# Optimization experiments

Measured on AMD Instinct MI355X. Metric: run time of the kernel, lower is better.

Reference implementation:

```python
import jax, jax.numpy as jnp
import numpy as np

C = 32          # mid_channel / in_channel
B = 8           # batch size (number of scenes)
N = 2_000_000   # total points across batch
BN_EPS = 1e-4   # BatchNorm1d eps from norm_fn


def setup_inputs() -> dict:
    key = jax.random.key(0)
    ks = jax.random.split(key, 8)
    s = 0.05
    return {
        "feats": jax.random.normal(ks[0], (N, C), dtype=jnp.float32),
        "batch_idxs": jnp.sort(jax.random.randint(ks[1], (N,), 0, B, dtype=jnp.int32)),
        "off_w1": jax.random.normal(ks[2], (C, C), dtype=jnp.float32) * s,
        "off_b1": jnp.zeros((C,), jnp.float32),
        "bn_gamma": jnp.ones((C,), jnp.float32),   # set_bn_init fills 1.0
        "bn_beta": jnp.zeros((C,), jnp.float32),   # set_bn_init fills 0.0
        "off_w2": jax.random.normal(ks[3], (C, 3), dtype=jnp.float32) * s,
        "off_b2": jnp.zeros((3,), jnp.float32),
        "mask_w1": jax.random.normal(ks[4], (C, C), dtype=jnp.float32) * s,
        "mask_b1": jnp.zeros((C,), jnp.float32),
        "mask_w2": jax.random.normal(ks[5], (C, 1), dtype=jnp.float32) * s,
        "mask_b2": jnp.zeros((1,), jnp.float32),
        "iou_w": jax.random.normal(ks[6], (C, 1), dtype=jnp.float32) * s,
        "iou_b": jnp.zeros((1,), jnp.float32),
    }


def reference(feats, batch_idxs, off_w1, off_b1, bn_gamma, bn_beta, off_w2, off_b2,
              mask_w1, mask_b1, mask_w2, mask_b2, iou_w, iou_b):
    # offset_linear = MLP([C, C, 3], norm_fn=BatchNorm1d): Linear -> BN -> ReLU -> Linear
    h = feats @ off_w1 + off_b1                      # [N, C]
    mu = h.mean(axis=0)
    var = jnp.mean(jnp.square(h - mu), axis=0)       # biased var (torch BN training fwd)
    h = (h - mu) * jax.lax.rsqrt(var + BN_EPS) * bn_gamma + bn_beta
    h = jax.nn.relu(h)
    pt_offsets = h @ off_w2 + off_b2                 # [N, 3]

    # mask_linear = MLP([C, C, 1], norm_fn=None): Linear -> ReLU -> Linear
    m = jax.nn.relu(feats @ mask_w1 + mask_b1)       # [N, C]
    mask_scores = m @ mask_w2 + mask_b2              # [N, 1]

    # global_pool: scatter mean of features over per-batch segments (batch offsets)
    ones = jnp.ones((feats.shape[0],), feats.dtype)
    counts = jax.ops.segment_sum(ones, batch_idxs, num_segments=B)          # [B]
    pooled = jax.ops.segment_sum(feats, batch_idxs, num_segments=B)         # [B, C]
    pooled = pooled / jnp.maximum(counts, 1.0)[:, None]

    # iou_score_linear on the pooled proposal feature
    iou_scores = pooled @ iou_w + iou_b              # [B, 1]
    return pt_offsets, mask_scores, pooled, iou_scores
```

## Files before the change

kernel.cpp:

```cpp
#include <hip/hip_runtime.h>

#define TPB 256

typedef __attribute__((ext_vector_type(8))) short short8;
typedef __attribute__((ext_vector_type(4))) float floatx4;

__device__ __forceinline__ unsigned short bf_trunc(float f){
    union { float f; unsigned u; } c; c.f = f;
    return (unsigned short)(c.u >> 16);
}
__device__ __forceinline__ unsigned short bf_rne(float f){
    union { float f; unsigned u; } c; c.f = f;
    unsigned r = c.u + 0x7fffu + ((c.u >> 16) & 1u);
    return (unsigned short)(r >> 16);
}
__device__ __forceinline__ unsigned pack_bf(float lo, float hi){
    union { float f; unsigned u; } a, b; a.f = lo; b.f = hi;
    return __builtin_amdgcn_perm(b.u, a.u, 0x07060302u);
}

__global__ __launch_bounds__(TPB, 4) void pass1_kernel(
    const float* __restrict__ feats, const int* __restrict__ bidx,
    const float* __restrict__ w1, const float* __restrict__ b1,
    const float* __restrict__ mw1, const float* __restrict__ mb1,
    const float* __restrict__ mw2, const float* __restrict__ mb2,
    float* __restrict__ mask_out,
    float* __restrict__ ws_sum, float* __restrict__ ws_sq,
    float* __restrict__ ws_pool, int N, int B)
{
    __shared__ float s_pool[8][32];
    __shared__ float s_sum[32];
    __shared__ float s_sq[32];
    __shared__ int   s_lb[9];

    const int tid  = threadIdx.x;
    const int lane = tid & 63;
    const int p = lane & 15;
    const int q = lane >> 4;

    if (tid < 32){ s_sum[tid] = 0.f; s_sq[tid] = 0.f; }
    ((float*)s_pool)[tid] = 0.f;
    if (tid <= B){
        int lo = 0, hi = N;
        while (lo < hi){
            const int mid = (lo + hi) >> 1;
            if (bidx[mid] < tid) lo = mid + 1; else hi = mid;
        }
        s_lb[tid] = lo;
    }
    __syncthreads();

    short8 aw0, aw1, am0, am1;
    floatx4 ci_h0, ci_h1, ci_m0, ci_m1;
    float mw2v[8];
#pragma unroll
    for (int j = 0; j < 8; ++j){
        const int k = q * 8 + j;
        aw0[j] = (short)bf_rne(w1 [k * 32 + p]);
        aw1[j] = (short)bf_rne(w1 [k * 32 + 16 + p]);
        am0[j] = (short)bf_rne(mw1[k * 32 + p]);
        am1[j] = (short)bf_rne(mw1[k * 32 + 16 + p]);
    }
#pragma unroll
    for (int r = 0; r < 4; ++r){
        const int c0 = q * 4 + r, c1 = 16 + q * 4 + r;
        ci_h0[r] = b1[c0];  ci_h1[r] = b1[c1];
        ci_m0[r] = mb1[c0]; ci_m1[r] = mb1[c1];
        mw2v[r] = mw2[c0];  mw2v[4 + r] = mw2[c1];
    }
    const float mb2s = mb2[0];

    float hsum[8] = {0,0,0,0,0,0,0,0};
    float hsq [8] = {0,0,0,0,0,0,0,0};
    float pacc[8] = {0,0,0,0,0,0,0,0};

    const int ntiles = (N + 15) >> 4;
    const int nw  = gridDim.x * (TPB / 64);
    const int wid = blockIdx.x * (TPB / 64) + (tid >> 6);

    int curb = 0;
    {
        const int r0 = wid << 4;
        while (curb < B - 1 && r0 >= s_lb[curb + 1]) curb++;
    }
    int lbn = s_lb[curb + 1];

    const size_t dstep = ((size_t)nw) << 9;
    const float* rp = feats + (((size_t)wid) << 9) + (p << 5) + (q << 3);

    floatx4 v0 = {0.f,0.f,0.f,0.f}, v1 = {0.f,0.f,0.f,0.f};
    if (wid < ntiles){
        if (((wid << 4) + p) < N){
            const floatx4* vp = (const floatx4*)rp;
            v0 = vp[0]; v1 = vp[1];
        }
    }

    for (int t = wid; t < ntiles; t += nw){
        floatx4 nv0 = {0.f,0.f,0.f,0.f}, nv1 = {0.f,0.f,0.f,0.f};
        const float* np = rp + dstep;
        if (t + nw < ntiles){
            if ((((t + nw) << 4) + p) < N){
                const floatx4* vp = (const floatx4*)np;
                nv0 = vp[0]; nv1 = vp[1];
            }
        }

        const int r0 = t << 4;
        if (r0 >= lbn){
#pragma unroll
            for (int j = 0; j < 8; ++j){
                if (pacc[j] != 0.f) atomicAdd(&s_pool[curb][q * 8 + j], pacc[j]);
                pacc[j] = 0.f;
            }
            do { curb++; } while (curb < B - 1 && r0 >= s_lb[curb + 1]);
            lbn = s_lb[curb + 1];
        }
        const bool slow = (r0 + 15 >= lbn);

        if (!slow){
            pacc[0] += v0[0]; pacc[1] += v0[1]; pacc[2] += v0[2]; pacc[3] += v0[3];
            pacc[4] += v1[0]; pacc[5] += v1[1]; pacc[6] += v1[2]; pacc[7] += v1[3];
        } else {
            const int row = r0 + p;
            if (row < N){
                int bl = curb;
                for (int c = curb + 1; c < B; ++c) bl += (row >= s_lb[c]);
                atomicAdd(&s_pool[bl][q * 8 + 0], v0[0]);
                atomicAdd(&s_pool[bl][q * 8 + 1], v0[1]);
                atomicAdd(&s_pool[bl][q * 8 + 2], v0[2]);
                atomicAdd(&s_pool[bl][q * 8 + 3], v0[3]);
                atomicAdd(&s_pool[bl][q * 8 + 4], v1[0]);
                atomicAdd(&s_pool[bl][q * 8 + 5], v1[1]);
                atomicAdd(&s_pool[bl][q * 8 + 6], v1[2]);
                atomicAdd(&s_pool[bl][q * 8 + 7], v1[3]);
            }
        }

        short8 bfrag;
        {
            unsigned* bw = (unsigned*)&bfrag;
            bw[0] = pack_bf(v0[0], v0[1]);
            bw[1] = pack_bf(v0[2], v0[3]);
            bw[2] = pack_bf(v1[0], v1[1]);
            bw[3] = pack_bf(v1[2], v1[3]);
        }

        const floatx4 ch0 = __builtin_amdgcn_mfma_f32_16x16x32_bf16(aw0, bfrag, ci_h0, 0, 0, 0);
        const floatx4 ch1 = __builtin_amdgcn_mfma_f32_16x16x32_bf16(aw1, bfrag, ci_h1, 0, 0, 0);
        const floatx4 cm0 = __builtin_amdgcn_mfma_f32_16x16x32_bf16(am0, bfrag, ci_m0, 0, 0, 0);
        const floatx4 cm1 = __builtin_amdgcn_mfma_f32_16x16x32_bf16(am1, bfrag, ci_m1, 0, 0, 0);

        if (!slow){
#pragma unroll
            for (int r = 0; r < 4; ++r){
                const float h0 = ch0[r]; hsum[r]     += h0; hsq[r]     = fmaf(h0, h0, hsq[r]);
                const float h1 = ch1[r]; hsum[4 + r] += h1; hsq[4 + r] = fmaf(h1, h1, hsq[4 + r]);
            }
        } else if (r0 + p < N){
#pragma unroll
            for (int r = 0; r < 4; ++r){
                const float h0 = ch0[r]; hsum[r]     += h0; hsq[r]     = fmaf(h0, h0, hsq[r]);
                const float h1 = ch1[r]; hsum[4 + r] += h1; hsq[4 + r] = fmaf(h1, h1, hsq[4 + r]);
            }
        }

        float tm = 0.f;
#pragma unroll
        for (int r = 0; r < 4; ++r){
            tm = fmaf(fmaxf(cm0[r], 0.f), mw2v[r],     tm);
            tm = fmaf(fmaxf(cm1[r], 0.f), mw2v[4 + r], tm);
        }
        tm += __shfl_xor(tm, 16, 64);
        tm += __shfl_xor(tm, 32, 64);
        if (q == 0 && (r0 + p) < N) mask_out[r0 + p] = tm + mb2s;

        v0 = nv0; v1 = nv1; rp = np;
    }

#pragma unroll
    for (int j = 0; j < 8; ++j){
        if (pacc[j] != 0.f) atomicAdd(&s_pool[curb][q * 8 + j], pacc[j]);
    }
#pragma unroll
    for (int i = 0; i < 8; ++i){
        const int ch = (i >> 2) * 16 + q * 4 + (i & 3);
        atomicAdd(&s_sum[ch], hsum[i]);
        atomicAdd(&s_sq[ch],  hsq[i]);
    }
    __syncthreads();
    if (tid < 32){
        atomicAdd(&ws_sum[tid], s_sum[tid]);
        atomicAdd(&ws_sq[tid],  s_sq[tid]);
    }
    {
        const float pv = ((float*)s_pool)[tid];
        if (pv != 0.f) atomicAdd(&ws_pool[tid], pv);
    }
}

__global__ __launch_bounds__(TPB, 4) void pass2_kernel(
    const float* __restrict__ feats, const int* __restrict__ bidx,
    const float* __restrict__ w1, const float* __restrict__ b1,
    const float* __restrict__ gamma, const float* __restrict__ beta,
    const float* __restrict__ w2, const float* __restrict__ b2,
    const float* __restrict__ iw, const float* __restrict__ ib,
    const float* __restrict__ ws_sum, const float* __restrict__ ws_sq,
    const float* __restrict__ ws_pool,
    float* __restrict__ pt_out, float* __restrict__ pooled_out,
    float* __restrict__ iou_out, int N, int B)
{
    __shared__ float s_sc[32];
    __shared__ float s_bp[32];
    __shared__ float s_pooled[256];
    __shared__ int   s_lb[33];

    const int tid  = threadIdx.x;
    const int lane = tid & 63;
    const int p = lane & 15;
    const int q = lane >> 4;

    if (tid < 32){
        const float invN = 1.f / (float)N;
        const float mu  = ws_sum[tid] * invN;
        const float var = ws_sq[tid] * invN - mu * mu;
        const float s   = gamma[tid] * rsqrtf(var + 1e-4f);
        s_sc[tid] = s;
        s_bp[tid] = (b1[tid] - mu) * s + beta[tid];
    }
    __syncthreads();

    if (blockIdx.x == 0){
        if (tid <= B){
            int lo = 0, hi = N;
            while (lo < hi){
                const int mid = (lo + hi) >> 1;
                if (bidx[mid] < tid) lo = mid + 1; else hi = mid;
            }
            s_lb[tid] = lo;
        }
        __syncthreads();
        if (tid < B * 32){
            const int bb = tid >> 5;
            const float cnt = fmaxf((float)(s_lb[bb + 1] - s_lb[bb]), 1.f);
            const float pv = ws_pool[tid] / cnt;
            s_pooled[tid]   = pv;
            pooled_out[tid] = pv;
        }
        __syncthreads();
        if (tid < B){
            float acc = ib[0];
#pragma unroll
            for (int i = 0; i < 32; ++i) acc = fmaf(s_pooled[tid * 32 + i], iw[i], acc);
            iou_out[tid] = acc;
        }
    }

    short8 pw0, pw1;
    floatx4 pc0, pc1;
    float w2v[24];
    const float sc0 = s_sc[p], sc1 = s_sc[16 + p];
#pragma unroll
    for (int j = 0; j < 8; ++j){
        const int k = q * 8 + j;
        pw0[j] = (short)bf_rne(w1[k * 32 + p]      * sc0);
        pw1[j] = (short)bf_rne(w1[k * 32 + 16 + p] * sc1);
    }
#pragma unroll
    for (int r = 0; r < 4; ++r){
        pc0[r] = s_bp[q * 4 + r];
        pc1[r] = s_bp[16 + q * 4 + r];
    }
#pragma unroll
    for (int i = 0; i < 8; ++i){
        const int ch = (i >> 2) * 16 + q * 4 + (i & 3);
        w2v[i]      = w2[ch * 3 + 0];
        w2v[8 + i]  = w2[ch * 3 + 1];
        w2v[16 + i] = w2[ch * 3 + 2];
    }
    const float b2v0 = b2[0], b2v1 = b2[1], b2v2 = b2[2];

    const int ntiles = (N + 15) >> 4;
    const int nw  = gridDim.x * (TPB / 64);
    const int wid = blockIdx.x * (TPB / 64) + (tid >> 6);

    const size_t dstep = ((size_t)nw) << 9;
    const float* rp = feats + (((size_t)wid) << 9) + (p << 5) + (q << 3);

    floatx4 v0 = {0.f,0.f,0.f,0.f}, v1 = {0.f,0.f,0.f,0.f};
    if (wid < ntiles){
        if (((wid << 4) + p) < N){
            const floatx4* vp = (const floatx4*)rp;
            v0 = vp[0]; v1 = vp[1];
        }
    }

    for (int t = wid; t < ntiles; t += nw){
        floatx4 nv0 = {0.f,0.f,0.f,0.f}, nv1 = {0.f,0.f,0.f,0.f};
        const float* np = rp + dstep;
        if (t + nw < ntiles){
            if ((((t + nw) << 4) + p) < N){
                const floatx4* vp = (const floatx4*)np;
                nv0 = vp[0]; nv1 = vp[1];
            }
        }

        short8 bfrag;
        {
            unsigned* bw = (unsigned*)&bfrag;
            bw[0] = pack_bf(v0[0], v0[1]);
            bw[1] = pack_bf(v0[2], v0[3]);
            bw[2] = pack_bf(v1[0], v1[1]);
            bw[3] = pack_bf(v1[2], v1[3]);
        }

        const floatx4 c0 = __builtin_amdgcn_mfma_f32_16x16x32_bf16(pw0, bfrag, pc0, 0, 0, 0);
        const floatx4 c1 = __builtin_amdgcn_mfma_f32_16x16x32_bf16(pw1, bfrag, pc1, 0, 0, 0);

        float s0 = 0.f, s1 = 0.f, s2 = 0.f;
#pragma unroll
        for (int r = 0; r < 4; ++r){
            const float p0 = fmaxf(c0[r], 0.f);
            const float p1 = fmaxf(c1[r], 0.f);
            s0 = fmaf(p0, w2v[r],      s0); s0 = fmaf(p1, w2v[4 + r],  s0);
            s1 = fmaf(p0, w2v[8 + r],  s1); s1 = fmaf(p1, w2v[12 + r], s1);
            s2 = fmaf(p0, w2v[16 + r], s2); s2 = fmaf(p1, w2v[20 + r], s2);
        }
        s0 += __shfl_xor(s0, 16, 64); s0 += __shfl_xor(s0, 32, 64);
        s1 += __shfl_xor(s1, 16, 64); s1 += __shfl_xor(s1, 32, 64);
        s2 += __shfl_xor(s2, 16, 64); s2 += __shfl_xor(s2, 32, 64);

        const int row = (t << 4) + p;
        if (lane < 48 && row < N){
            float val = (q == 0) ? (s0 + b2v0) : ((q == 1) ? (s1 + b2v1) : (s2 + b2v2));
            pt_out[(size_t)(t << 4) * 3 + p * 3 + q] = val;
        }

        v0 = nv0; v1 = nv1; rp = np;
    }
}

extern "C" void kernel_launch(void* const* d_in, const int* in_sizes, int n_in,
                              void* d_out, int out_size, void* d_ws, size_t ws_size,
                              hipStream_t stream) {
    const float* feats = (const float*)d_in[0];
    const int*   bidx  = (const int*)d_in[1];
    const float* w1    = (const float*)d_in[2];
    const float* b1    = (const float*)d_in[3];
    const float* gamma = (const float*)d_in[4];
    const float* beta  = (const float*)d_in[5];
    const float* w2    = (const float*)d_in[6];
    const float* b2    = (const float*)d_in[7];
    const float* mw1   = (const float*)d_in[8];
    const float* mb1   = (const float*)d_in[9];
    const float* mw2   = (const float*)d_in[10];
    const float* mb2   = (const float*)d_in[11];
    const float* iw    = (const float*)d_in[12];
    const float* ib    = (const float*)d_in[13];

    const int N = in_sizes[0] / 32;
    const int B = (out_size - 4 * N) / 33;

    float* out    = (float*)d_out;
    float* pt     = out;
    float* mask   = out + (size_t)3 * N;
    float* pooled = out + (size_t)4 * N;
    float* iou    = pooled + (size_t)B * 32;

    float* ws      = (float*)d_ws;
    float* ws_sum  = ws;
    float* ws_sq   = ws + 32;
    float* ws_pool = ws + 64;

    hipMemsetAsync(ws, 0, (size_t)(64 + B * 32) * sizeof(float), stream);

    int dev = 0;
    hipGetDevice(&dev);
    hipDeviceProp_t prop;
    hipGetDeviceProperties(&prop, dev);
    int per1 = 0, per2 = 0;
    hipOccupancyMaxActiveBlocksPerMultiprocessor(&per1, pass1_kernel, TPB, 0);
    hipOccupancyMaxActiveBlocksPerMultiprocessor(&per2, pass2_kernel, TPB, 0);
    int g1 = per1 * prop.multiProcessorCount; if (g1 < 256) g1 = 256;
    int g2 = per2 * prop.multiProcessorCount; if (g2 < 256) g2 = 256;

    pass1_kernel<<<g1, TPB, 0, stream>>>(feats, bidx, w1, b1, mw1, mb1, mw2, mb2,
                                         mask, ws_sum, ws_sq, ws_pool, N, B);
    pass2_kernel<<<g2, TPB, 0, stream>>>(feats, bidx, w1, b1, gamma, beta, w2, b2,
                                         iw, ib, ws_sum, ws_sq, ws_pool,
                                         pt, pooled, iou, N, B);
}
```

Measured before the change: 468.0 us.

## Process two 16-row tiles per iteration over contiguous per-wave ranges with fixed grid

Each wave now owns a contiguous range of 32-row pairs instead of grid-striding 16-row tiles, and handles two tiles per loop iteration with eight (pass1) or four (pass2) independent MFMAs. This gives more memory and compute work in flight per iteration and better locality, and the fixed 1024-block grid removes the per-call device property and occupancy queries from the host launch path. Launch bounds drop to 2 blocks per CU to leave room for the extra registers. The cost is fewer resident waves and a grid size no longer tuned to the device.

```diff
diff --git a/kernel.cpp b/kernel.cpp
--- a/kernel.cpp
+++ b/kernel.cpp
@@ -1,14 +1,11 @@
 #include <hip/hip_runtime.h>
 
 #define TPB 256
+#define GRID_BLOCKS 1024
 
 typedef __attribute__((ext_vector_type(8))) short short8;
 typedef __attribute__((ext_vector_type(4))) float floatx4;
 
-__device__ __forceinline__ unsigned short bf_trunc(float f){
-    union { float f; unsigned u; } c; c.f = f;
-    return (unsigned short)(c.u >> 16);
-}
 __device__ __forceinline__ unsigned short bf_rne(float f){
     union { float f; unsigned u; } c; c.f = f;
     unsigned r = c.u + 0x7fffu + ((c.u >> 16) & 1u);
@@ -19,7 +16,7 @@
     return __builtin_amdgcn_perm(b.u, a.u, 0x07060302u);
 }
 
-__global__ __launch_bounds__(TPB, 4) void pass1_kernel(
+__global__ __launch_bounds__(TPB, 2) void pass1_kernel(
     const float* __restrict__ feats, const int* __restrict__ bidx,
     const float* __restrict__ w1, const float* __restrict__ b1,
     const float* __restrict__ mw1, const float* __restrict__ mb1,
@@ -74,39 +71,38 @@
     float hsq [8] = {0,0,0,0,0,0,0,0};
     float pacc[8] = {0,0,0,0,0,0,0,0};
 
-    const int ntiles = (N + 15) >> 4;
+    const int npairs = (N + 31) >> 5;
     const int nw  = gridDim.x * (TPB / 64);
     const int wid = blockIdx.x * (TPB / 64) + (tid >> 6);
+    const int g0  = (int)((long)wid       * npairs / nw);
+    const int g1  = (int)((long)(wid + 1) * npairs / nw);
 
     int curb = 0;
     {
-        const int r0 = wid << 4;
+        const int r0 = g0 << 5;
         while (curb < B - 1 && r0 >= s_lb[curb + 1]) curb++;
     }
     int lbn = s_lb[curb + 1];
 
-    const size_t dstep = ((size_t)nw) << 9;
-    const float* rp = feats + (((size_t)wid) << 9) + (p << 5) + (q << 3);
-
-    floatx4 v0 = {0.f,0.f,0.f,0.f}, v1 = {0.f,0.f,0.f,0.f};
-    if (wid < ntiles){
-        if (((wid << 4) + p) < N){
-            const floatx4* vp = (const floatx4*)rp;
-            v0 = vp[0]; v1 = vp[1];
-        }
-    }
-
-    for (int t = wid; t < ntiles; t += nw){
-        floatx4 nv0 = {0.f,0.f,0.f,0.f}, nv1 = {0.f,0.f,0.f,0.f};
-        const float* np = rp + dstep;
-        if (t + nw < ntiles){
-            if ((((t + nw) << 4) + p) < N){
-                const floatx4* vp = (const floatx4*)np;
-                nv0 = vp[0]; nv1 = vp[1];
-            }
-        }
-
-        const int r0 = t << 4;
+    const float* rp = feats + (((size_t)g0) << 10) + (p << 5) + (q << 3);
+
+    floatx4 vA0 = {0,0,0,0}, vA1 = {0,0,0,0}, vB0 = {0,0,0,0}, vB1 = {0,0,0,0};
+    if (g0 < g1){
+        const int rA = (g0 << 5) + p;
+        if (rA < N){ const floatx4* vp = (const floatx4*)rp; vA0 = vp[0]; vA1 = vp[1]; }
+        if (rA + 16 < N){ const floatx4* vp = (const floatx4*)(rp + 512); vB0 = vp[0]; vB1 = vp[1]; }
+    }
+
+    for (int g = g0; g < g1; ++g){
+        floatx4 nA0 = {0,0,0,0}, nA1 = {0,0,0,0}, nB0 = {0,0,0,0}, nB1 = {0,0,0,0};
+        const float* np = rp + 1024;
+        if (g + 1 < g1){
+            const int rA = ((g + 1) << 5) + p;
+            if (rA < N){ const floatx4* vp = (const floatx4*)np; nA0 = vp[0]; nA1 = vp[1]; }
+            if (rA + 16 < N){ const floatx4* vp = (const floatx4*)(np + 512); nB0 = vp[0]; nB1 = vp[1]; }
+        }
+
+        const int r0 = g << 5;
         if (r0 >= lbn){
 #pragma unroll
             for (int j = 0; j < 8; ++j){
@@ -116,66 +112,101 @@
             do { curb++; } while (curb < B - 1 && r0 >= s_lb[curb + 1]);
             lbn = s_lb[curb + 1];
         }
-        const bool slow = (r0 + 15 >= lbn);
+        const bool slow = (r0 + 31 >= lbn) || (r0 + 31 >= N);
 
         if (!slow){
-            pacc[0] += v0[0]; pacc[1] += v0[1]; pacc[2] += v0[2]; pacc[3] += v0[3];
-            pacc[4] += v1[0]; pacc[5] += v1[1]; pacc[6] += v1[2]; pacc[7] += v1[3];
+            pacc[0] += vA0[0] + vB0[0]; pacc[1] += vA0[1] + vB0[1];
+            pacc[2] += vA0[2] + vB0[2]; pacc[3] += vA0[3] + vB0[3];
+            pacc[4] += vA1[0] + vB1[0]; pacc[5] += vA1[1] + vB1[1];
+            pacc[6] += vA1[2] + vB1[2]; pacc[7] += vA1[3] + vB1[3];
         } else {
-            const int row = r0 + p;
-            if (row < N){
+            const int rA = r0 + p, rB = r0 + 16 + p;
+            if (rA < N){
                 int bl = curb;
-                for (int c = curb + 1; c < B; ++c) bl += (row >= s_lb[c]);
-                atomicAdd(&s_pool[bl][q * 8 + 0], v0[0]);
-                atomicAdd(&s_pool[bl][q * 8 + 1], v0[1]);
-                atomicAdd(&s_pool[bl][q * 8 + 2], v0[2]);
-                atomicAdd(&s_pool[bl][q * 8 + 3], v0[3]);
-                atomicAdd(&s_pool[bl][q * 8 + 4], v1[0]);
-                atomicAdd(&s_pool[bl][q * 8 + 5], v1[1]);
-                atomicAdd(&s_pool[bl][q * 8 + 6], v1[2]);
-                atomicAdd(&s_pool[bl][q * 8 + 7], v1[3]);
-            }
-        }
-
-        short8 bfrag;
+                for (int c = curb + 1; c < B; ++c) bl += (rA >= s_lb[c]);
+                atomicAdd(&s_pool[bl][q * 8 + 0], vA0[0]);
+                atomicAdd(&s_pool[bl][q * 8 + 1], vA0[1]);
+                atomicAdd(&s_pool[bl][q * 8 + 2], vA0[2]);
+                atomicAdd(&s_pool[bl][q * 8 + 3], vA0[3]);
+                atomicAdd(&s_pool[bl][q * 8 + 4], vA1[0]);
+                atomicAdd(&s_pool[bl][q * 8 + 5], vA1[1]);
+                atomicAdd(&s_pool[bl][q * 8 + 6], vA1[2]);
+                atomicAdd(&s_pool[bl][q * 8 + 7], vA1[3]);
+            }
+            if (rB < N){
+                int bl = curb;
+                for (int c = curb + 1; c < B; ++c) bl += (rB >= s_lb[c]);
+                atomicAdd(&s_pool[bl][q * 8 + 0], vB0[0]);
+                atomicAdd(&s_pool[bl][q * 8 + 1], vB0[1]);
+                atomicAdd(&s_pool[bl][q * 8 + 2], vB0[2]);
+                atomicAdd(&s_pool[bl][q * 8 + 3], vB0[3]);
+                atomicAdd(&s_pool[bl][q * 8 + 4], vB1[0]);
+                atomicAdd(&s_pool[bl][q * 8 + 5], vB1[1]);
+                atomicAdd(&s_pool[bl][q * 8 + 6], vB1[2]);
+                atomicAdd(&s_pool[bl][q * 8 + 7], vB1[3]);
+            }
+        }
+
+        short8 bfA, bfB;
         {
-            unsigned* bw = (unsigned*)&bfrag;
-            bw[0] = pack_bf(v0[0], v0[1]);
-            bw[1] = pack_bf(v0[2], v0[3]);
-            bw[2] = pack_bf(v1[0], v1[1]);
-            bw[3] = pack_bf(v1[2], v1[3]);
-        }
-
-        const floatx4 ch0 = __builtin_amdgcn_mfma_f32_16x16x32_bf16(aw0, bfrag, ci_h0, 0, 0, 0);
-        const floatx4 ch1 = __builtin_amdgcn_mfma_f32_16x16x32_bf16(aw1, bfrag, ci_h1, 0, 0, 0);
-        const floatx4 cm0 = __builtin_amdgcn_mfma_f32_16x16x32_bf16(am0, bfrag, ci_m0, 0, 0, 0);
-        const floatx4 cm1 = __builtin_amdgcn_mfma_f32_16x16x32_bf16(am1, bfrag, ci_m1, 0, 0, 0);
+            unsigned* ba = (unsigned*)&bfA;
+            ba[0] = pack_bf(vA0[0], vA0[1]); ba[1] = pack_bf(vA0[2], vA0[3]);
+            ba[2] = pack_bf(vA1[0], vA1[1]); ba[3] = pack_bf(vA1[2], vA1[3]);
+            unsigned* bb = (unsigned*)&bfB;
+            bb[0] = pack_bf(vB0[0], vB0[1]); bb[1] = pack_bf(vB0[2], vB0[3]);
+            bb[2] = pack_bf(vB1[0], vB1[1]); bb[3] = pack_bf(vB1[2], vB1[3]);
+        }
+
+        const floatx4 chA0 = __builtin_amdgcn_mfma_f32_16x16x32_bf16(aw0, bfA, ci_h0, 0, 0, 0);
+        const floatx4 chA1 = __builtin_amdgcn_mfma_f32_16x16x32_bf16(aw1, bfA, ci_h1, 0, 0, 0);
+        const floatx4 cmA0 = __builtin_amdgcn_mfma_f32_16x16x32_bf16(am0, bfA, ci_m0, 0, 0, 0);
+        const floatx4 cmA1 = __builtin_amdgcn_mfma_f32_16x16x32_bf16(am1, bfA, ci_m1, 0, 0, 0);
+        const floatx4 chB0 = __builtin_amdgcn_mfma_f32_16x16x32_bf16(aw0, bfB, ci_h0, 0, 0, 0);
+        const floatx4 chB1 = __builtin_amdgcn_mfma_f32_16x16x32_bf16(aw1, bfB, ci_h1, 0, 0, 0);
+        const floatx4 cmB0 = __builtin_amdgcn_mfma_f32_16x16x32_bf16(am0, bfB, ci_m0, 0, 0, 0);
+        const floatx4 cmB1 = __builtin_amdgcn_mfma_f32_16x16x32_bf16(am1, bfB, ci_m1, 0, 0, 0);
 
         if (!slow){
 #pragma unroll
             for (int r = 0; r < 4; ++r){
-                const float h0 = ch0[r]; hsum[r]     += h0; hsq[r]     = fmaf(h0, h0, hsq[r]);
-                const float h1 = ch1[r]; hsum[4 + r] += h1; hsq[4 + r] = fmaf(h1, h1, hsq[4 + r]);
-            }
-        } else if (r0 + p < N){
-#pragma unroll
-            for (int r = 0; r < 4; ++r){
-                const float h0 = ch0[r]; hsum[r]     += h0; hsq[r]     = fmaf(h0, h0, hsq[r]);
-                const float h1 = ch1[r]; hsum[4 + r] += h1; hsq[4 + r] = fmaf(h1, h1, hsq[4 + r]);
-            }
-        }
-
-        float tm = 0.f;
+                const float a0 = chA0[r], b0 = chB0[r];
+                hsum[r] += a0 + b0;
+                hsq [r] = fmaf(a0, a0, fmaf(b0, b0, hsq[r]));
+                const float a1 = chA1[r], b1v = chB1[r];
+                hsum[4 + r] += a1 + b1v;
+                hsq [4 + r] = fmaf(a1, a1, fmaf(b1v, b1v, hsq[4 + r]));
+            }
+        } else {
+            if (r0 + p < N){
+#pragma unroll
+                for (int r = 0; r < 4; ++r){
+                    const float a0 = chA0[r]; hsum[r]     += a0; hsq[r]     = fmaf(a0, a0, hsq[r]);
+                    const float a1 = chA1[r]; hsum[4 + r] += a1; hsq[4 + r] = fmaf(a1, a1, hsq[4 + r]);
+                }
+            }
+            if (r0 + 16 + p < N){
+#pragma unroll
+                for (int r = 0; r < 4; ++r){
+                    const float b0 = chB0[r]; hsum[r]     += b0; hsq[r]     = fmaf(b0, b0, hsq[r]);
+                    const float b1v = chB1[r]; hsum[4 + r] += b1v; hsq[4 + r] = fmaf(b1v, b1v, hsq[4 + r]);
+                }
+            }
+        }
+
+        float tmA = 0.f, tmB = 0.f;
 #pragma unroll
         for (int r = 0; r < 4; ++r){
-            tm = fmaf(fmaxf(cm0[r], 0.f), mw2v[r],     tm);
-            tm = fmaf(fmaxf(cm1[r], 0.f), mw2v[4 + r], tm);
-        }
-        tm += __shfl_xor(tm, 16, 64);
-        tm += __shfl_xor(tm, 32, 64);
-        if (q == 0 && (r0 + p) < N) mask_out[r0 + p] = tm + mb2s;
-
-        v0 = nv0; v1 = nv1; rp = np;
+            tmA = fmaf(fmaxf(cmA0[r], 0.f), mw2v[r],     tmA);
+            tmA = fmaf(fmaxf(cmA1[r], 0.f), mw2v[4 + r], tmA);
+            tmB = fmaf(fmaxf(cmB0[r], 0.f), mw2v[r],     tmB);
+            tmB = fmaf(fmaxf(cmB1[r], 0.f), mw2v[4 + r], tmB);
+        }
+        tmA += __shfl_xor(tmA, 16, 64); tmA += __shfl_xor(tmA, 32, 64);
+        tmB += __shfl_xor(tmB, 16, 64); tmB += __shfl_xor(tmB, 32, 64);
+        if (q == 0 && (r0 + p) < N)      mask_out[r0 + p]      = tmA + mb2s;
+        if (q == 0 && (r0 + 16 + p) < N) mask_out[r0 + 16 + p] = tmB + mb2s;
+
+        vA0 = nA0; vA1 = nA1; vB0 = nB0; vB1 = nB1; rp = np;
     }
 
 #pragma unroll
@@ -199,7 +230,7 @@
     }
 }
 
-__global__ __launch_bounds__(TPB, 4) void pass2_kernel(
+__global__ __launch_bounds__(TPB, 2) void pass2_kernel(
     const float* __restrict__ feats, const int* __restrict__ bidx,
     const float* __restrict__ w1, const float* __restrict__ b1,
     const float* __restrict__ gamma, const float* __restrict__ beta,
@@ -280,63 +311,78 @@
     }
     const float b2v0 = b2[0], b2v1 = b2[1], b2v2 = b2[2];
 
-    const int ntiles = (N + 15) >> 4;
+    const int npairs = (N + 31) >> 5;
     const int nw  = gridDim.x * (TPB / 64);
     const int wid = blockIdx.x * (TPB / 64) + (tid >> 6);
-
-    const size_t dstep = ((size_t)nw) << 9;
-    const float* rp = feats + (((size_t)wid) << 9) + (p << 5) + (q << 3);
-
-    floatx4 v0 = {0.f,0.f,0.f,0.f}, v1 = {0.f,0.f,0.f,0.f};
-    if (wid < ntiles){
-        if (((wid << 4) + p) < N){
-            const floatx4* vp = (const floatx4*)rp;
-            v0 = vp[0]; v1 = vp[1];
-        }
-    }
-
-    for (int t = wid; t < ntiles; t += nw){
-        floatx4 nv0 = {0.f,0.f,0.f,0.f}, nv1 = {0.f,0.f,0.f,0.f};
-        const float* np = rp + dstep;
-        if (t + nw < ntiles){
-            if ((((t + nw) << 4) + p) < N){
-                const floatx4* vp = (const floatx4*)np;
-                nv0 = vp[0]; nv1 = vp[1];
-            }
-        }
-
-        short8 bfrag;
+    const int g0  = (int)((long)wid       * npairs / nw);
+    const int g1  = (int)((long)(wid + 1) * npairs / nw);
+
+    const float* rp = feats + (((size_t)g0) << 10) + (p << 5) + (q << 3);
+
+    floatx4 vA0 = {0,0,0,0}, vA1 = {0,0,0,0}, vB0 = {0,0,0,0}, vB1 = {0,0,0,0};
+    if (g0 < g1){
+        const int rA = (g0 << 5) + p;
+        if (rA < N){ const floatx4* vp = (const floatx4*)rp; vA0 = vp[0]; vA1 = vp[1]; }
+        if (rA + 16 < N){ const floatx4* vp = (const floatx4*)(rp + 512); vB0 = vp[0]; vB1 = vp[1]; }
+    }
+
+    for (int g = g0; g < g1; ++g){
+        floatx4 nA0 = {0,0,0,0}, nA1 = {0,0,0,0}, nB0 = {0,0,0,0}, nB1 = {0,0,0,0};
+        const float* np = rp + 1024;
+        if (g + 1 < g1){
+            const int rA = ((g + 1) << 5) + p;
+            if (rA < N){ const floatx4* vp = (const floatx4*)np; nA0 = vp[0]; nA1 = vp[1]; }
+            if (rA + 16 < N){ const floatx4* vp = (const floatx4*)(np + 512); nB0 = vp[0]; nB1 = vp[1]; }
+        }
+
+        short8 bfA, bfB;
         {
-            unsigned* bw = (unsigned*)&bfrag;
-            bw[0] = pack_bf(v0[0], v0[1]);
-            bw[1] = pack_bf(v0[2], v0[3]);
-            bw[2] = pack_bf(v1[0], v1[1]);
-            bw[3] = pack_bf(v1[2], v1[3]);
-        }
-
-        const floatx4 c0 = __builtin_amdgcn_mfma_f32_16x16x32_bf16(pw0, bfrag, pc0, 0, 0, 0);
-        const floatx4 c1 = __builtin_amdgcn_mfma_f32_16x16x32_bf16(pw1, bfrag, pc1, 0, 0, 0);
-
-        float s0 = 0.f, s1 = 0.f, s2 = 0.f;
+            unsigned* ba = (unsigned*)&bfA;
+            ba[0] = pack_bf(vA0[0], vA0[1]); ba[1] = pack_bf(vA0[2], vA0[3]);
+            ba[2] = pack_bf(vA1[0], vA1[1]); ba[3] = pack_bf(vA1[2], vA1[3]);
+            unsigned* bb = (unsigned*)&bfB;
+            bb[0] = pack_bf(vB0[0], vB0[1]); bb[1] = pack_bf(vB0[2], vB0[3]);
+            bb[2] = pack_bf(vB1[0], vB1[1]); bb[3] = pack_bf(vB1[2], vB1[3]);
+        }
+
+        const floatx4 cA0 = __builtin_amdgcn_mfma_f32_16x16x32_bf16(pw0, bfA, pc0, 0, 0, 0);
+        const floatx4 cA1 = __builtin_amdgcn_mfma_f32_16x16x32_bf16(pw1, bfA, pc1, 0, 0, 0);
+        const floatx4 cB0 = __builtin_amdgcn_mfma_f32_16x16x32_bf16(pw0, bfB, pc0, 0, 0, 0);
+        const floatx4 cB1 = __builtin_amdgcn_mfma_f32_16x16x32_bf16(pw1, bfB, pc1, 0, 0, 0);
+
+        float sA0 = 0.f, sA1 = 0.f, sA2 = 0.f, sB0 = 0.f, sB1 = 0.f, sB2 = 0.f;
 #pragma unroll
         for (int r = 0; r < 4; ++r){
-            const float p0 = fmaxf(c0[r], 0.f);
-            const float p1 = fmaxf(c1[r], 0.f);
-            s0 = fmaf(p0, w2v[r],      s0); s0 = fmaf(p1, w2v[4 + r],  s0);
-            s1 = fmaf(p0, w2v[8 + r],  s1); s1 = fmaf(p1, w2v[12 + r], s1);
-            s2 = fmaf(p0, w2v[16 + r], s2); s2 = fmaf(p1, w2v[20 + r], s2);
-        }
-        s0 += __shfl_xor(s0, 16, 64); s0 += __shfl_xor(s0, 32, 64);
-        s1 += __shfl_xor(s1, 16, 64); s1 += __shfl_xor(s1, 32, 64);
-        s2 += __shfl_xor(s2, 16, 64); s2 += __shfl_xor(s2, 32, 64);
-
-        const int row = (t << 4) + p;
-        if (lane < 48 && row < N){
-            float val = (q == 0) ? (s0 + b2v0) : ((q == 1) ? (s1 + b2v1) : (s2 + b2v2));
-            pt_out[(size_t)(t << 4) * 3 + p * 3 + q] = val;
-        }
-
-        v0 = nv0; v1 = nv1; rp = np;
+            const float a0 = fmaxf(cA0[r], 0.f);
+            const float a1 = fmaxf(cA1[r], 0.f);
+            sA0 = fmaf(a0, w2v[r],      sA0); sA0 = fmaf(a1, w2v[4 + r],  sA0);
+            sA1 = fmaf(a0, w2v[8 + r],  sA1); sA1 = fmaf(a1, w2v[12 + r], sA1);
+            sA2 = fmaf(a0, w2v[16 + r], sA2); sA2 = fmaf(a1, w2v[20 + r], sA2);
+            const float b0 = fmaxf(cB0[r], 0.f);
+            const float b1v = fmaxf(cB1[r], 0.f);
+            sB0 = fmaf(b0, w2v[r],      sB0); sB0 = fmaf(b1v, w2v[4 + r],  sB0);
+            sB1 = fmaf(b0, w2v[8 + r],  sB1); sB1 = fmaf(b1v, w2v[12 + r], sB1);
+            sB2 = fmaf(b0, w2v[16 + r], sB2); sB2 = fmaf(b1v, w2v[20 + r], sB2);
+        }
+        sA0 += __shfl_xor(sA0, 16, 64); sA0 += __shfl_xor(sA0, 32, 64);
+        sA1 += __shfl_xor(sA1, 16, 64); sA1 += __shfl_xor(sA1, 32, 64);
+        sA2 += __shfl_xor(sA2, 16, 64); sA2 += __shfl_xor(sA2, 32, 64);
+        sB0 += __shfl_xor(sB0, 16, 64); sB0 += __shfl_xor(sB0, 32, 64);
+        sB1 += __shfl_xor(sB1, 16, 64); sB1 += __shfl_xor(sB1, 32, 64);
+        sB2 += __shfl_xor(sB2, 16, 64); sB2 += __shfl_xor(sB2, 32, 64);
+
+        const int r0 = g << 5;
+        const int rA = r0 + p, rB = r0 + 16 + p;
+        if (lane < 48 && rA < N){
+            float val = (q == 0) ? (sA0 + b2v0) : ((q == 1) ? (sA1 + b2v1) : (sA2 + b2v2));
+            pt_out[(size_t)rA * 3 + q] = val;
+        }
+        if (lane < 48 && rB < N){
+            float val = (q == 0) ? (sB0 + b2v0) : ((q == 1) ? (sB1 + b2v1) : (sB2 + b2v2));
+            pt_out[(size_t)rB * 3 + q] = val;
+        }
+
+        vA0 = nA0; vA1 = nA1; vB0 = nB0; vB1 = nB1; rp = np;
     }
 }
 
@@ -374,19 +420,9 @@
 
     hipMemsetAsync(ws, 0, (size_t)(64 + B * 32) * sizeof(float), stream);
 
-    int dev = 0;
-    hipGetDevice(&dev);
-    hipDeviceProp_t prop;
-    hipGetDeviceProperties(&prop, dev);
-    int per1 = 0, per2 = 0;
-    hipOccupancyMaxActiveBlocksPerMultiprocessor(&per1, pass1_kernel, TPB, 0);
-    hipOccupancyMaxActiveBlocksPerMultiprocessor(&per2, pass2_kernel, TPB, 0);
-    int g1 = per1 * prop.multiProcessorCount; if (g1 < 256) g1 = 256;
-    int g2 = per2 * prop.multiProcessorCount; if (g2 < 256) g2 = 256;
-
-    pass1_kernel<<<g1, TPB, 0, stream>>>(feats, bidx, w1, b1, mw1, mb1, mw2, mb2,
-                                         mask, ws_sum, ws_sq, ws_pool, N, B);
-    pass2_kernel<<<g2, TPB, 0, stream>>>(feats, bidx, w1, b1, gamma, beta, w2, b2,
-                                         iw, ib, ws_sum, ws_sq, ws_pool,
-                                         pt, pooled, iou, N, B);
+    pass1_kernel<<<GRID_BLOCKS, TPB, 0, stream>>>(feats, bidx, w1, b1, mw1, mb1, mw2, mb2,
+                                                  mask, ws_sum, ws_sq, ws_pool, N, B);
+    pass2_kernel<<<GRID_BLOCKS, TPB, 0, stream>>>(feats, bidx, w1, b1, gamma, beta, w2, b2,
+                                                  iw, ib, ws_sum, ws_sq, ws_pool,
+                                                  pt, pooled, iou, N, B);
 }
```

New measurement: 480.9 us. +2.8%, slower.
